# Optimization experiments

Measured on AMD Instinct MI355X. Metric: run time of the kernel, lower is better.

The kernel has to match this reference:

```python
import jax, jax.numpy as jnp
import numpy as np

N = 50000      # nodes
E = 800000     # edges (avg degree 16)
IN = 128       # input feature dim
D = 128        # embed dim (heads=1, concat)
SLOPE = 0.2    # GATv2Conv default negative_slope


def setup_inputs() -> dict:
    key = jax.random.key(0)
    ks = jax.random.split(key, 16)
    s_in = 1.0 / np.sqrt(IN)
    s_d = 1.0 / np.sqrt(D)
    inp = {
        "node_fts": jax.random.normal(ks[0], (N, IN), dtype=jnp.float32),
        "edge_index": jax.random.randint(ks[1], (2, E), 0, N, dtype=jnp.int64),
        # layer 1 (in_dim -> embed_dim)
        "Wl1": jax.random.normal(ks[2], (IN, D), dtype=jnp.float32) * s_in,
        "bl1": jnp.zeros((D,), dtype=jnp.float32),
        "Wr1": jax.random.normal(ks[3], (IN, D), dtype=jnp.float32) * s_in,
        "br1": jnp.zeros((D,), dtype=jnp.float32),
        "att1": jax.random.normal(ks[4], (D,), dtype=jnp.float32) * s_d,
        "bias1": jnp.zeros((D,), dtype=jnp.float32),
        # layer 2 (embed_dim -> embed_dim)
        "Wl2": jax.random.normal(ks[5], (D, D), dtype=jnp.float32) * s_d,
        "bl2": jnp.zeros((D,), dtype=jnp.float32),
        "Wr2": jax.random.normal(ks[6], (D, D), dtype=jnp.float32) * s_d,
        "br2": jnp.zeros((D,), dtype=jnp.float32),
        "att2": jax.random.normal(ks[7], (D,), dtype=jnp.float32) * s_d,
        "bias2": jnp.zeros((D,), dtype=jnp.float32),
    }
    return inp


def gatv2_layer(x, src, dst, Wl, bl, Wr, br, att, bias):
    # GATv2Conv (heads=1, share_weights=False):
    #   x_j (source message features) = lin_l(x), x_i (target) = lin_r(x)
    xl = x @ Wl + bl                                      # [N, D]
    xr = x @ Wr + br                                      # [N, D]
    e = jax.nn.leaky_relu(xl[src] + xr[dst], SLOPE)       # [E, D]
    logits = e @ att                                      # [E]
    # softmax over incoming edges of each target node
    m = jax.ops.segment_max(logits, dst, num_segments=N)  # [N], -inf for isolated
    m = jnp.where(jnp.isneginf(m), 0.0, m)
    a = jnp.exp(logits - m[dst])                          # [E]
    s = jax.ops.segment_sum(a, dst, num_segments=N)       # [N]
    a = a / jnp.maximum(s[dst], 1e-16)
    out = jax.ops.segment_sum(a[:, None] * xl[src], dst, num_segments=N)  # [N, D]
    return out + bias


def reference(node_fts, edge_index,
              Wl1, bl1, Wr1, br1, att1, bias1,
              Wl2, bl2, Wr2, br2, att2, bias2):
    src, dst = edge_index[0], edge_index[1]
    x = jax.nn.relu(gatv2_layer(node_fts, src, dst, Wl1, bl1, Wr1, br1, att1, bias1))
    x = jax.nn.relu(gatv2_layer(x, src, dst, Wl2, bl2, Wr2, br2, att2, bias2))
    return x
```

## Files before the change

kernel.cpp:

```cpp
#include <hip/hip_runtime.h>
#include <hip/hip_bf16.h>
#include <hip/hip_fp16.h>

#define N_NODES 50000
#define N_EDGES 800000
#define DIM 128
#define NGROUPS (N_NODES / 16)
#define LROW2 132
#define KBUCKET 196
#define BCAP 5120
#define EPB 4000

typedef __attribute__((ext_vector_type(8))) _Float16 hfrag8;
typedef __attribute__((ext_vector_type(4))) float f32x4;
typedef _Float16 h2 __attribute__((ext_vector_type(2)));

__device__ __forceinline__ h2 u2h(uint u){ union{uint u; h2 h;} c; c.u = u; return c.h; }


__global__ __launch_bounds__(256) void bucket_scatter_k(
    const int* __restrict__ src, const int* __restrict__ dst,
    int* __restrict__ bucket_cnt, uint2* __restrict__ bucketdata)
{
  __shared__ int cnt[KBUCKET], base[KBUCKET], cur[KBUCKET];
  int tid = threadIdx.x;
  for (int t = tid; t < KBUCKET; t += 256) { cnt[t] = 0; cur[t] = 0; }
  __syncthreads();
  int e0 = blockIdx.x * EPB;
  for (int i = tid; i < EPB; i += 256)
    atomicAdd(&cnt[dst[e0 + i] >> 8], 1);
  __syncthreads();
  for (int t = tid; t < KBUCKET; t += 256)
    base[t] = atomicAdd(&bucket_cnt[t], cnt[t]);
  __syncthreads();
  for (int i = tid; i < EPB; i += 256) {
    int s = src[e0 + i], d = dst[e0 + i];
    int b = d >> 8;
    int r = atomicAdd(&cur[b], 1);
    bucketdata[(size_t)b * BCAP + base[b] + r] = make_uint2((uint)s, (uint)d);
  }
}

__global__ __launch_bounds__(256) void bucket_csr_k(
    const int* __restrict__ bucket_cnt, const uint2* __restrict__ bucketdata,
    int* __restrict__ row_start, int* __restrict__ csr_src)
{
  __shared__ int hist[256], cur[256];
  __shared__ int wsumA[4], wsumB[4];
  int b = blockIdx.x, tid = threadIdx.x;
  int lane = tid & 63, w = tid >> 6;
  int vv = (tid < b) ? bucket_cnt[tid] : 0;
  #pragma unroll
  for (int off = 32; off > 0; off >>= 1) vv += __shfl_xor(vv, off, 64);
  if (lane == 0) wsumA[w] = vv;
  hist[tid] = 0;
  __syncthreads();
  int base_csr = wsumA[0] + wsumA[1] + wsumA[2] + wsumA[3];
  int cnt = bucket_cnt[b];
  int node0 = b << 8;
  const uint2* bd = bucketdata + (size_t)b * BCAP;
  for (int i = tid; i < cnt; i += 256)
    atomicAdd(&hist[bd[i].y & 255], 1);
  __syncthreads();
  int v = hist[tid];
  int inc = v;
  #pragma unroll
  for (int off = 1; off < 64; off <<= 1) {
    int y = __shfl_up(inc, off, 64);
    if (lane >= off) inc += y;
  }
  if (lane == 63) wsumB[w] = inc;
  __syncthreads();
  int wpre = 0;
  #pragma unroll
  for (int i = 0; i < 4; i++) if (i < w) wpre += wsumB[i];
  int excl = wpre + inc - v;
  int node = node0 + tid;
  if (node < N_NODES) row_start[node] = base_csr + excl;
  if (b == 0 && tid == 0) row_start[N_NODES] = N_EDGES;
  cur[tid] = excl;
  __syncthreads();
  for (int i = tid; i < cnt; i += 256) {
    uint2 p = bd[i];
    int r = atomicAdd(&cur[p.y & 255], 1);
    csr_src[base_csr + r] = (int)p.x;
  }
}

__global__ __launch_bounds__(64) void prep_w(
    const float* __restrict__ Wl1, const float* __restrict__ Wr1,
    const float* __restrict__ Wl2, const float* __restrict__ Wr2,
    _Float16* __restrict__ wb)
{
  int bid = blockIdx.x;
  int layer = bid >> 6, rest = bid & 63;
  int C = rest >> 4, g = rest & 15;
  int lane = threadIdx.x;
  int m = lane & 15, q = lane >> 4;
  int dim = g*16 + m;
  const float* W = layer ? (dim < 128 ? Wl2 : Wr2) : (dim < 128 ? Wl1 : Wr1);
  int dcol = dim & 127;
  _Float16 h[8];
  #pragma unroll
  for (int j = 0; j < 8; j++) {
    int k = C*32 + q*8 + j;
    h[j] = (_Float16)W[(size_t)k*DIM + dcol];
  }
  size_t off = ((size_t)bid*64 + lane)*8;
  *(hfrag8*)(wb + off) = *(hfrag8*)h;
}

template<typename TIN>
__global__ __launch_bounds__(256) void gemm_mfma(
    const TIN* __restrict__ x,
    const _Float16* __restrict__ wb,
    const float* __restrict__ bl, const float* __restrict__ br,
    __half* __restrict__ xlh, __half* __restrict__ xrh)
{
  __shared__ float lds[4][16*LROW2];
  int wv = threadIdx.x >> 6, lane = threadIdx.x & 63;
  int G = blockIdx.x * 4 + wv;
  if (G >= NGROUPS) return;

  int m = lane & 15, q = lane >> 4;
  const TIN* xrow = x + (size_t)(G*16 + m)*DIM + q*8;

  f32x4 acc[16];
  #pragma unroll
  for (int g = 0; g < 16; g++) acc[g] = (f32x4)(0.f);

  #pragma unroll 1
  for (int C = 0; C < 4; C++) {
    hfrag8 ah;
    if constexpr (sizeof(TIN) == 4) {
      float v[8];
      *(float4*)(v)     = *(const float4*)((const float*)xrow + C*32);
      *(float4*)(v + 4) = *(const float4*)((const float*)xrow + C*32 + 4);
      _Float16 hh[8];
      #pragma unroll
      for (int j = 0; j < 8; j++) hh[j] = (_Float16)v[j];
      ah = *(hfrag8*)hh;
    } else {
      ah = *(const hfrag8*)((const _Float16*)xrow + C*32);
    }
    #pragma unroll
    for (int g = 0; g < 16; g++) {
      size_t boff = ((size_t)(C*16 + g)*64 + lane)*8;
      hfrag8 bh = *(const hfrag8*)(wb + boff);
      acc[g] = __builtin_amdgcn_mfma_f32_16x16x32_f16(ah, bh, acc[g], 0, 0, 0);
    }
  }

  float* wlds = lds[wv];
  int dcol = (lane & 31) * 4;
  int rowsel = lane >> 5;
  #pragma unroll
  for (int half = 0; half < 2; half++) {
    #pragma unroll
    for (int g = 0; g < 8; g++) {
      #pragma unroll
      for (int r = 0; r < 4; r++)
        wlds[(q*4 + r)*LROW2 + g*16 + m] = acc[half*8 + g][r];
    }
    const float* B = half ? br : bl;
    ushort* outh = half ? (ushort*)xrh : (ushort*)xlh;
    float4 bv = *(const float4*)(B + dcol);
    #pragma unroll
    for (int it = 0; it < 8; it++) {
      int i = it*2 + rowsel;
      float4 vv = *(const float4*)(wlds + i*LROW2 + dcol);
      int node = G*16 + i;
      __half2 h0 = __floats2half2_rn(vv.x + bv.x, vv.y + bv.y);
      __half2 h1 = __floats2half2_rn(vv.z + bv.z, vv.w + bv.w);
      uint2 pk = make_uint2(*(uint*)&h0, *(uint*)&h1);
      *(uint2*)(outh + (size_t)node*DIM + dcol) = pk;
    }
  }
}

template<int OUT>
__global__ __launch_bounds__(256) void gat_gather(
    const __half* __restrict__ xlh, const __half* __restrict__ xrh,
    const int* __restrict__ row_start, const int* __restrict__ csr_src,
    const float* __restrict__ att, const float* __restrict__ bias,
    float* __restrict__ outf, __half* __restrict__ outh)
{
  int wave = (blockIdx.x * 256 + threadIdx.x) >> 6;
  int lane = threadIdx.x & 63;
  int q4 = lane >> 4;
  int hl = lane & 15;
  int node = wave * 4 + q4;
  int r0 = row_start[node];
  int deg = row_start[node + 1] - r0;
  int last = r0 + deg - 1;
  int d1 = max(deg, __shfl_xor(deg, 16, 64));
  int dmax = max(d1, __shfl_xor(d1, 32, 64));

  uint4 rx = *(const uint4*)((const ushort*)xrh + (size_t)node*DIM + hl*8);
  h2 xr01 = u2h(rx.x), xr23 = u2h(rx.y), xr45 = u2h(rx.z), xr67 = u2h(rx.w);
  const float* ap = att + hl*8;
  float4 af0 = *(const float4*)(ap);
  float4 af1 = *(const float4*)(ap + 4);
  h2 a01 = {(_Float16)af0.x, (_Float16)af0.y};
  h2 a23 = {(_Float16)af0.z, (_Float16)af0.w};
  h2 a45 = {(_Float16)af1.x, (_Float16)af1.y};
  h2 a67 = {(_Float16)af1.z, (_Float16)af1.w};
  const h2 c02 = {(_Float16)0.2f, (_Float16)0.2f};

  float l = 0.f;
  float b0a=0,b1a=0,b2a=0,b3a=0,b4a=0,b5a=0,b6a=0,b7a=0;
  const ushort* xbase = (const ushort*)xlh + hl*8;

  for (int t = 0; t < dmax; t += 4) {
    uint4 raw[4];
    #pragma unroll
    for (int j = 0; j < 4; j++) {
      int rr = r0 + t + j;
      int rc = rr <= last ? rr : last;
      rc = rc >= 0 ? rc : 0;
      int si = csr_src[rc];
      raw[j] = *(const uint4*)(xbase + (size_t)si*DIM);
    }
    #pragma unroll
    for (int j = 0; j < 4; j++) {
      h2 v01 = u2h(raw[j].x), v23 = u2h(raw[j].y);
      h2 v45 = u2h(raw[j].z), v67 = u2h(raw[j].w);
      h2 s01 = v01 + xr01, s23 = v23 + xr23;
      h2 s45 = v45 + xr45, s67 = v67 + xr67;
      s01 = __builtin_elementwise_max(s01, s01 * c02);
      s23 = __builtin_elementwise_max(s23, s23 * c02);
      s45 = __builtin_elementwise_max(s45, s45 * c02);
      s67 = __builtin_elementwise_max(s67, s67 * c02);
      float p = __builtin_amdgcn_fdot2(s01, a01, 0.f, false);
      p = __builtin_amdgcn_fdot2(s23, a23, p, false);
      p = __builtin_amdgcn_fdot2(s45, a45, p, false);
      p = __builtin_amdgcn_fdot2(s67, a67, p, false);
      #pragma unroll
      for (int o = 1; o <= 8; o <<= 1) p += __shfl_xor(p, o, 64);
      float w = (t + j < deg) ? __expf(p) : 0.f;
      l += w;
      b0a = fmaf(w, (float)v01.x, b0a); b1a = fmaf(w, (float)v01.y, b1a);
      b2a = fmaf(w, (float)v23.x, b2a); b3a = fmaf(w, (float)v23.y, b3a);
      b4a = fmaf(w, (float)v45.x, b4a); b5a = fmaf(w, (float)v45.y, b5a);
      b6a = fmaf(w, (float)v67.x, b6a); b7a = fmaf(w, (float)v67.y, b7a);
    }
  }

  float inv = 1.f / fmaxf(l, 1e-16f);
  const float* bp = bias + hl*8;
  float4 c0 = *(const float4*)(bp);
  float4 c1 = *(const float4*)(bp + 4);
  float4 o0, o1;
  o0.x = fmaxf(fmaf(b0a, inv, c0.x), 0.f);
  o0.y = fmaxf(fmaf(b1a, inv, c0.y), 0.f);
  o0.z = fmaxf(fmaf(b2a, inv, c0.z), 0.f);
  o0.w = fmaxf(fmaf(b3a, inv, c0.w), 0.f);
  o1.x = fmaxf(fmaf(b4a, inv, c1.x), 0.f);
  o1.y = fmaxf(fmaf(b5a, inv, c1.y), 0.f);
  o1.z = fmaxf(fmaf(b6a, inv, c1.z), 0.f);
  o1.w = fmaxf(fmaf(b7a, inv, c1.w), 0.f);
  if (OUT == 0) {
    float* op = outf + (size_t)node*DIM + hl*8;
    *(float4*)(op)     = o0;
    *(float4*)(op + 4) = o1;
  } else {
    __half2 h0 = __floats2half2_rn(o0.x, o0.y);
    __half2 h1 = __floats2half2_rn(o0.z, o0.w);
    __half2 h2v = __floats2half2_rn(o1.x, o1.y);
    __half2 h3 = __floats2half2_rn(o1.z, o1.w);
    uint4 pk = make_uint4(*(uint*)&h0, *(uint*)&h1, *(uint*)&h2v, *(uint*)&h3);
    *(uint4*)((ushort*)outh + (size_t)node*DIM + hl*8) = pk;
  }
}

extern "C" void kernel_launch(void* const* d_in, const int* in_sizes, int n_in,
                              void* d_out, int out_size, void* d_ws, size_t ws_size,
                              hipStream_t stream)
{
  const float* node_fts = (const float*)d_in[0];
  const int*  edge_index = (const int*)d_in[1];
  const float* Wl1 = (const float*)d_in[2];
  const float* bl1 = (const float*)d_in[3];
  const float* Wr1 = (const float*)d_in[4];
  const float* br1 = (const float*)d_in[5];
  const float* att1 = (const float*)d_in[6];
  const float* bias1 = (const float*)d_in[7];
  const float* Wl2 = (const float*)d_in[8];
  const float* bl2 = (const float*)d_in[9];
  const float* Wr2 = (const float*)d_in[10];
  const float* br2 = (const float*)d_in[11];
  const float* att2 = (const float*)d_in[12];
  const float* bias2 = (const float*)d_in[13];
  const int* src = edge_index;
  const int* dst = edge_index + N_EDGES;

  char* ws = (char*)d_ws;
  __half* xlh = (__half*)ws;               ws += (size_t)N_NODES*DIM*2;
  __half* xrh = (__half*)ws;               ws += (size_t)N_NODES*DIM*2;
  __half* hh  = (__half*)ws;               ws += (size_t)N_NODES*DIM*2;
  _Float16* wb = (_Float16*)ws;            ws += 2*4*16*64*8*2;
  int* row_start   = (int*)ws;             ws += (N_NODES+1)*4;
  int* csr_src     = (int*)ws;             ws += (size_t)N_EDGES*4;
  int* bucket_cnt  = (int*)ws;             ws += KBUCKET*4;
  uint2* bucketdata = (uint2*)ws;          ws += (size_t)KBUCKET*BCAP*8;

  const int W_LAYER = 4*16*64*8;

  int gemm_blocks = (NGROUPS + 3) / 4;
  int gather_blocks = N_NODES / 16;

  hipMemsetAsync(bucket_cnt, 0, KBUCKET * sizeof(int), stream);
  bucket_scatter_k<<<N_EDGES/EPB, 256, 0, stream>>>(src, dst, bucket_cnt, bucketdata);
  bucket_csr_k<<<KBUCKET, 256, 0, stream>>>(bucket_cnt, bucketdata, row_start, csr_src);

  prep_w<<<128, 64, 0, stream>>>(Wl1, Wr1, Wl2, Wr2, wb);

  gemm_mfma<float><<<gemm_blocks, 256, 0, stream>>>(node_fts, wb, bl1, br1, xlh, xrh);
  gat_gather<1><<<gather_blocks, 256, 0, stream>>>(xlh, xrh, row_start, csr_src,
                                                   att1, bias1, nullptr, hh);
  gemm_mfma<_Float16><<<gemm_blocks, 256, 0, stream>>>((const _Float16*)hh,
                                             wb + W_LAYER, bl2, br2, xlh, xrh);
  gat_gather<0><<<gather_blocks, 256, 0, stream>>>(xlh, xrh, row_start, csr_src,
                                                   att2, bias2, (float*)d_out, nullptr);
}
```

Measured before the change: 250.7 us.

## Pack bucket entries, fold memset into prep, widen per-node gather batching

Packs each bucketed edge into one 32-bit word (src shifted left by 8, plus the low 8 bits of dst), halving the intermediate traffic in the CSR build. Halves the edges handled per scatter block. Replaces the host memset with a zeroing step inside prep_w, which now runs first. The gather loop now runs to each node's own degree rather than the wave-wide maximum, and issues 8 index loads and then 8 feature loads per step, to raise memory-level parallelism and cut wasted iterations. The risks are more register pressure from the 8-wide batch and divergence between the four nodes sharing a wave.

```diff
diff --git a/kernel.cpp b/kernel.cpp
--- a/kernel.cpp
+++ b/kernel.cpp
@@ -9,7 +9,7 @@
 #define LROW2 132
 #define KBUCKET 196
 #define BCAP 5120
-#define EPB 4000
+#define EPB 2000
 
 typedef __attribute__((ext_vector_type(8))) _Float16 hfrag8;
 typedef __attribute__((ext_vector_type(4))) float f32x4;
@@ -20,7 +20,7 @@
 
 __global__ __launch_bounds__(256) void bucket_scatter_k(
     const int* __restrict__ src, const int* __restrict__ dst,
-    int* __restrict__ bucket_cnt, uint2* __restrict__ bucketdata)
+    int* __restrict__ bucket_cnt, uint* __restrict__ bucketdata)
 {
   __shared__ int cnt[KBUCKET], base[KBUCKET], cur[KBUCKET];
   int tid = threadIdx.x;
@@ -37,12 +37,12 @@
     int s = src[e0 + i], d = dst[e0 + i];
     int b = d >> 8;
     int r = atomicAdd(&cur[b], 1);
-    bucketdata[(size_t)b * BCAP + base[b] + r] = make_uint2((uint)s, (uint)d);
+    bucketdata[(size_t)b * BCAP + base[b] + r] = ((uint)s << 8) | (uint)(d & 255);
   }
 }
 
 __global__ __launch_bounds__(256) void bucket_csr_k(
-    const int* __restrict__ bucket_cnt, const uint2* __restrict__ bucketdata,
+    const int* __restrict__ bucket_cnt, const uint* __restrict__ bucketdata,
     int* __restrict__ row_start, int* __restrict__ csr_src)
 {
   __shared__ int hist[256], cur[256];
@@ -58,9 +58,9 @@
   int base_csr = wsumA[0] + wsumA[1] + wsumA[2] + wsumA[3];
   int cnt = bucket_cnt[b];
   int node0 = b << 8;
-  const uint2* bd = bucketdata + (size_t)b * BCAP;
+  const uint* bd = bucketdata + (size_t)b * BCAP;
   for (int i = tid; i < cnt; i += 256)
-    atomicAdd(&hist[bd[i].y & 255], 1);
+    atomicAdd(&hist[bd[i] & 255], 1);
   __syncthreads();
   int v = hist[tid];
   int inc = v;
@@ -81,18 +81,21 @@
   cur[tid] = excl;
   __syncthreads();
   for (int i = tid; i < cnt; i += 256) {
-    uint2 p = bd[i];
-    int r = atomicAdd(&cur[p.y & 255], 1);
-    csr_src[base_csr + r] = (int)p.x;
+    uint p = bd[i];
+    int r = atomicAdd(&cur[p & 255], 1);
+    csr_src[base_csr + r] = (int)(p >> 8);
   }
 }
 
 __global__ __launch_bounds__(64) void prep_w(
     const float* __restrict__ Wl1, const float* __restrict__ Wr1,
     const float* __restrict__ Wl2, const float* __restrict__ Wr2,
-    _Float16* __restrict__ wb)
+    _Float16* __restrict__ wb, int* __restrict__ bucket_cnt)
 {
   int bid = blockIdx.x;
+  if (bid == 0) {
+    for (int t = threadIdx.x; t < KBUCKET; t += 64) bucket_cnt[t] = 0;
+  }
   int layer = bid >> 6, rest = bid & 63;
   int C = rest >> 4, g = rest & 15;
   int lane = threadIdx.x;
@@ -193,8 +196,6 @@
   int r0 = row_start[node];
   int deg = row_start[node + 1] - r0;
   int last = r0 + deg - 1;
-  int d1 = max(deg, __shfl_xor(deg, 16, 64));
-  int dmax = max(d1, __shfl_xor(d1, 32, 64));
 
   uint4 rx = *(const uint4*)((const ushort*)xrh + (size_t)node*DIM + hl*8);
   h2 xr01 = u2h(rx.x), xr23 = u2h(rx.y), xr45 = u2h(rx.z), xr67 = u2h(rx.w);
@@ -211,18 +212,19 @@
   float b0a=0,b1a=0,b2a=0,b3a=0,b4a=0,b5a=0,b6a=0,b7a=0;
   const ushort* xbase = (const ushort*)xlh + hl*8;
 
-  for (int t = 0; t < dmax; t += 4) {
-    uint4 raw[4];
-    #pragma unroll
-    for (int j = 0; j < 4; j++) {
+  for (int t = 0; t < deg; t += 8) {
+    int idx[8];
+    #pragma unroll
+    for (int j = 0; j < 8; j++) {
       int rr = r0 + t + j;
-      int rc = rr <= last ? rr : last;
-      rc = rc >= 0 ? rc : 0;
-      int si = csr_src[rc];
-      raw[j] = *(const uint4*)(xbase + (size_t)si*DIM);
-    }
-    #pragma unroll
-    for (int j = 0; j < 4; j++) {
+      idx[j] = csr_src[rr <= last ? rr : last];
+    }
+    uint4 raw[8];
+    #pragma unroll
+    for (int j = 0; j < 8; j++)
+      raw[j] = *(const uint4*)(xbase + (size_t)idx[j]*DIM);
+    #pragma unroll
+    for (int j = 0; j < 8; j++) {
       h2 v01 = u2h(raw[j].x), v23 = u2h(raw[j].y);
       h2 v45 = u2h(raw[j].z), v67 = u2h(raw[j].w);
       h2 s01 = v01 + xr01, s23 = v23 + xr23;
@@ -302,18 +304,17 @@
   int* row_start   = (int*)ws;             ws += (N_NODES+1)*4;
   int* csr_src     = (int*)ws;             ws += (size_t)N_EDGES*4;
   int* bucket_cnt  = (int*)ws;             ws += KBUCKET*4;
-  uint2* bucketdata = (uint2*)ws;          ws += (size_t)KBUCKET*BCAP*8;
+  uint* bucketdata = (uint*)ws;            ws += (size_t)KBUCKET*BCAP*4;
 
   const int W_LAYER = 4*16*64*8;
 
   int gemm_blocks = (NGROUPS + 3) / 4;
   int gather_blocks = N_NODES / 16;
 
-  hipMemsetAsync(bucket_cnt, 0, KBUCKET * sizeof(int), stream);
+  prep_w<<<128, 64, 0, stream>>>(Wl1, Wr1, Wl2, Wr2, wb, bucket_cnt);
+
   bucket_scatter_k<<<N_EDGES/EPB, 256, 0, stream>>>(src, dst, bucket_cnt, bucketdata);
   bucket_csr_k<<<KBUCKET, 256, 0, stream>>>(bucket_cnt, bucketdata, row_start, csr_src);
-
-  prep_w<<<128, 64, 0, stream>>>(Wl1, Wr1, Wl2, Wr2, wb);
 
   gemm_mfma<float><<<gemm_blocks, 256, 0, stream>>>(node_fts, wb, bl1, br1, xlh, xrh);
   gat_gather<1><<<gather_blocks, 256, 0, stream>>>(xlh, xrh, row_start, csr_src,
```

New measurement: 248.2 us. Within noise of the previous version (-1.0%).
